# Kernel tuning notes

Measured on AMD Instinct MI355X. Metric: run time of the kernel, lower is better.

The kernel has to match this reference:

```python
import jax, jax.numpy as jnp
import numpy as np

B, C, H, W = 16, 128, 64, 64
NH = 8
HD = C // NH          # head dim == pos_embed_dim
WIN = 5               # relative-position window
OUT = 512             # out_dim of the final 1x1 projection


def _dwconv(x, w, pad):
    """Depthwise 2D conv, x: (N, Cin, H, W), w: (Cin, 1, kh, kw)."""
    return jax.lax.conv_general_dilated(
        x, w, window_strides=(1, 1), padding=[(pad, pad), (pad, pad)],
        dimension_numbers=('NCHW', 'OIHW', 'NCHW'),
        feature_group_count=x.shape[1])


def setup_inputs() -> dict:
    key = jax.random.key(0)
    ks = jax.random.split(key, 6)
    src = jax.random.normal(ks[0], (B, C, H, W), jnp.float32)
    cpe_w = jax.random.normal(ks[1], (C, 1, 3, 3), jnp.float32) * 0.1
    qkv_w = jax.random.normal(ks[2], (3 * C, C), jnp.float32) * (1.0 / np.sqrt(C))
    rel_pos = jax.random.normal(ks[3], (HD, WIN, WIN), jnp.float32) * 0.02
    conv1d_w = jax.random.normal(ks[4], (3,), jnp.float32) * 0.5
    out_w = jax.random.normal(ks[5], (OUT, 2 * C), jnp.float32) * (1.0 / np.sqrt(2 * C))
    return dict(src=src, cpe_w=cpe_w, qkv_w=qkv_w, rel_pos=rel_pos,
                conv1d_w=conv1d_w, out_w=out_w)


def reference(src, cpe_w, qkv_w, rel_pos, conv1d_w, out_w):
    scaling = HD ** (-0.5)
    feature_raw = src

    # CPE: depthwise 3x3 conv residual
    s = _dwconv(src, cpe_w, 1) + src

    # 1x1 QKV conv == channel GEMM
    qkv = jnp.einsum('oc,bchw->bohw', qkv_w, s)          # (B, 3C, H, W)
    q, k, v = jnp.split(qkv, 3, axis=1)                  # each (B, C, H, W)

    q = q.reshape(B * NH, HD, H, W)
    k = k.reshape(B * NH, HD, H, W)
    v = v.reshape(B * NH, HD, H, W)

    N = H * W
    kf = jax.nn.softmax(k.reshape(B * NH, HD, N), axis=-1)   # softmax over spatial
    vf = v.reshape(B * NH, HD, N)
    content_lambda = jnp.einsum('bin,bon->bio', kf, vf)      # (B*NH, HD, HD)
    qf = q.reshape(B * NH, HD, N) * scaling
    content_output = jnp.einsum('bin,bio->bon', qf, content_lambda)
    content_output = content_output.reshape(B * NH, HD, H, W)

    # relative-position lambda: depthwise 5x5 conv of v with rel_pos_embed
    position_lambda = _dwconv(v, rel_pos[:, None, :, :], WIN // 2)
    position_output = q * position_lambda

    result1 = (content_output + position_output).reshape(B, C, H, W)

    # ECA-style channel attention on the raw input
    pool = jnp.mean(feature_raw, axis=(2, 3))                # (B, C)
    xp = jnp.pad(pool, ((0, 0), (1, 1)))
    ca = jax.nn.sigmoid(conv1d_w[0] * xp[:, :-2]
                        + conv1d_w[1] * xp[:, 1:-1]
                        + conv1d_w[2] * xp[:, 2:])           # (B, C)
    result2 = feature_raw * ca[:, :, None, None]

    cat = jnp.concatenate([result1, result2], axis=1)       # (B, 2C, H, W)
    return jnp.einsum('oc,bchw->bohw', out_w, cat)           # (B, OUT, H, W)
```

## Files before the change

### kernel.cpp

```cpp
#include <hip/hip_runtime.h>
#include <hip/hip_bf16.h>
#include <math.h>

#define Bb   16
#define Cc   128
#define Hh   64
#define Wwid 64
#define Nn   4096
#define NHh  8
#define HDd  16
#define BHh  128
#define TCc  384
#define OUTc 512
#define KK2  256

typedef _Float16 f16x8 __attribute__((ext_vector_type(8)));
typedef float    f32x4 __attribute__((ext_vector_type(4)));

__device__ __forceinline__ ushort f2h_bits(float f) {
    _Float16 h = (_Float16)f;
    ushort u;
    __builtin_memcpy(&u, &h, 2);
    return u;
}
__device__ __forceinline__ float h2f_bits(ushort u) {
    _Float16 h;
    __builtin_memcpy(&h, &u, 2);
    return (float)h;
}

__global__ void cvt_weights(const float* __restrict__ a, int na,
                            const float* __restrict__ b2, int nb,
                            ushort* __restrict__ ya, ushort* __restrict__ yb) {
    int i = blockIdx.x * 256 + threadIdx.x;
    if (i < na) ya[i] = f2h_bits(a[i]);
    else if (i < na + nb) yb[i - na] = f2h_bits(b2[i - na]);
}

__global__ void __launch_bounds__(256) cpe_pool_kernel(const float* __restrict__ src,
                                                       const float* __restrict__ cpe_w,
                                                       ushort* __restrict__ s,
                                                       float* __restrict__ pool) {
    int bc = blockIdx.x;
    int c  = bc & (Cc - 1);
    const float* sp = src + (size_t)bc * Nn;
    __shared__ float pl[66 * 66];
    __shared__ float red[256];
    int t = threadIdx.x;
    for (int i = t; i < 66 * 66; i += 256) pl[i] = 0.f;
    __syncthreads();
    float lsum = 0.f;
    for (int i = t; i < Nn / 4; i += 256) {
        float4 v4 = ((const float4*)sp)[i];
        lsum += v4.x + v4.y + v4.z + v4.w;
        int e = i * 4, y = e >> 6, x = e & 63;
        float* d = &pl[(y + 1) * 66 + x + 1];
        d[0] = v4.x; d[1] = v4.y; d[2] = v4.z; d[3] = v4.w;
    }
    red[t] = lsum;
    float w[9];
#pragma unroll
    for (int k = 0; k < 9; k++) w[k] = cpe_w[c * 9 + k];
    __syncthreads();
    for (int s2 = 128; s2 > 0; s2 >>= 1) {
        if (t < s2) red[t] += red[t + s2];
        __syncthreads();
    }
    if (t == 0) pool[bc] = red[0] * (1.0f / Nn);
    int x = t & 63, ys = (t >> 6) * 16;
    float r[3][3];
#pragma unroll
    for (int k = 0; k < 2; k++)
#pragma unroll
        for (int j = 0; j < 3; j++) r[k][j] = pl[(ys + k) * 66 + x + j];
    ushort* dst = s + (size_t)bc * Nn;
#pragma unroll
    for (int yy = 0; yy < 16; yy++) {
        int y = ys + yy;
#pragma unroll
        for (int j = 0; j < 3; j++) r[2][j] = pl[(y + 2) * 66 + x + j];
        float acc = r[1][1];
#pragma unroll
        for (int k = 0; k < 3; k++)
#pragma unroll
            for (int j = 0; j < 3; j++) acc += r[k][j] * w[k * 3 + j];
        dst[y * 64 + x] = f2h_bits(acc);
#pragma unroll
        for (int j = 0; j < 3; j++) { r[0][j] = r[1][j]; r[1][j] = r[2][j]; }
    }
}

__global__ void ca_kernel(const float* __restrict__ pool,
                          const float* __restrict__ w3,
                          float* __restrict__ ca) {
    int i = blockIdx.x * 256 + threadIdx.x;
    if (i >= Bb * Cc) return;
    int c = i & (Cc - 1);
    float left  = (c == 0)        ? 0.f : pool[i - 1];
    float mid   = pool[i];
    float right = (c == Cc - 1)   ? 0.f : pool[i + 1];
    float v = w3[0] * left + w3[1] * mid + w3[2] * right;
    ca[i] = 1.f / (1.f + expf(-v));
}

__global__ void transpose_s(const ushort* __restrict__ s, ushort* __restrict__ sT) {
    int bz = blockIdx.z;
    int c0 = blockIdx.y * 64;
    int n0 = blockIdx.x * 64;
    __shared__ ushort t[64][68];
    int nn = threadIdx.x & 63, c4 = threadIdx.x >> 6;
    const ushort* sp = s + ((size_t)bz * Cc + c0) * Nn + n0;
#pragma unroll
    for (int p = 0; p < 16; p++) {
        int cc = p * 4 + c4;
        t[cc][nn] = sp[(size_t)cc * Nn + nn];
    }
    __syncthreads();
    int cw = threadIdx.x & 63, n4 = threadIdx.x >> 6;
    ushort* dp = sT + ((size_t)bz * Nn + n0) * Cc + c0;
#pragma unroll
    for (int p = 0; p < 16; p++) {
        int n = p * 4 + n4;
        dp[(size_t)n * Cc + cw] = t[cw][n];
    }
}

template<int K, int M>
__global__ void __launch_bounds__(256) gemm_tn(const ushort* __restrict__ A,
                                               const ushort* __restrict__ Bt,
                                               float* __restrict__ C) {
    const int bz = blockIdx.z;
    const int m0 = blockIdx.y * 128;
    const int n0 = blockIdx.x * 128;
    __shared__ __align__(16) ushort Al[128 * 32];
    __shared__ __align__(16) ushort Bl[128 * 32];
    const int tid  = threadIdx.x;
    const int wave = tid >> 6, lane = tid & 63;
    const int r = lane & 15, q = lane >> 4;
    const int wr = wave >> 1, wc = wave & 1;

    const ushort* Ag = A + (size_t)m0 * K;
    const ushort* Bg = Bt + ((size_t)bz * Nn + n0) * K;

    f32x4 acc[4][4] = {};

    for (int k0 = 0; k0 < K; k0 += 32) {
#pragma unroll
        for (int p = 0; p < 2; p++) {
            int seg = p * 4 + wave;
            int idx = seg * 64 + lane;
            int row = idx >> 2, ch = idx & 3;
            const ushort* ga = Ag + (size_t)row * K + k0 + ch * 8;
            const ushort* gb = Bg + (size_t)row * K + k0 + ch * 8;
            __builtin_amdgcn_global_load_lds(
                (const __attribute__((address_space(1))) void*)(const void*)ga,
                (__attribute__((address_space(3))) void*)(void*)(Al + seg * 512),
                16, 0, 0);
            __builtin_amdgcn_global_load_lds(
                (const __attribute__((address_space(1))) void*)(const void*)gb,
                (__attribute__((address_space(3))) void*)(void*)(Bl + seg * 512),
                16, 0, 0);
        }
        __syncthreads();

        const ushort* Apt = Al + (size_t)(wr * 64 + r) * 32 + q * 8;
        const ushort* Bpt = Bl + (size_t)(wc * 64 + r) * 32 + q * 8;
        f16x8 af[4], bf[4];
#pragma unroll
        for (int i = 0; i < 4; i++) af[i] = *(const f16x8*)(Apt + i * 16 * 32);
#pragma unroll
        for (int j = 0; j < 4; j++) bf[j] = *(const f16x8*)(Bpt + j * 16 * 32);
#pragma unroll
        for (int i = 0; i < 4; i++)
#pragma unroll
            for (int j = 0; j < 4; j++)
                acc[i][j] = __builtin_amdgcn_mfma_f32_16x16x32_f16(af[i], bf[j], acc[i][j], 0, 0, 0);
        __syncthreads();
    }

    float* Cp = C + ((size_t)bz * M + m0 + wr * 64) * Nn + n0 + wc * 64;
#pragma unroll
    for (int i = 0; i < 4; i++)
#pragma unroll
        for (int j = 0; j < 4; j++)
#pragma unroll
            for (int e = 0; e < 4; e++)
                Cp[(size_t)(i * 16 + q * 4 + e) * Nn + j * 16 + r] = acc[i][j][e];
}

__global__ void krowstat(const float* __restrict__ qkv,
                         float* __restrict__ mx, float* __restrict__ irs) {
    int row = blockIdx.x;
    int b = row >> 7, c = row & (Cc - 1);
    const float* p = qkv + (size_t)b * TCc * Nn + (size_t)(Cc + c) * Nn;
    int t = threadIdx.x;
    __shared__ float red[256];
    float m = -1e30f;
    float vals[16];
#pragma unroll
    for (int j = 0; j < 16; j++) {
        vals[j] = p[t + j * 256];
        m = fmaxf(m, vals[j]);
    }
    red[t] = m; __syncthreads();
    for (int s2 = 128; s2 > 0; s2 >>= 1) {
        if (t < s2) red[t] = fmaxf(red[t], red[t + s2]);
        __syncthreads();
    }
    m = red[0]; __syncthreads();
    float sum = 0.f;
#pragma unroll
    for (int j = 0; j < 16; j++) sum += __expf(vals[j] - m);
    red[t] = sum; __syncthreads();
    for (int s2 = 128; s2 > 0; s2 >>= 1) {
        if (t < s2) red[t] += red[t + s2];
        __syncthreads();
    }
    if (t == 0) { mx[row] = m; irs[row] = 1.f / red[0]; }
}

__global__ void __launch_bounds__(256) lambda_mfma(const float* __restrict__ qkv,
                                                   const float* __restrict__ mx,
                                                   const float* __restrict__ irs,
                                                   float* __restrict__ lamP) {
    int bh   = blockIdx.x >> 1;
    int half = blockIdx.x & 1;
    int b = bh >> 3, h = bh & 7;
    int wave = threadIdx.x >> 6, lane = threadIdx.x & 63;
    int r = lane & 15, q = lane >> 4;
    const float* kf = qkv + (size_t)b * TCc * Nn + (size_t)(Cc + h * HDd) * Nn;
    const float* vf = qkv + (size_t)b * TCc * Nn + (size_t)(2 * Cc + h * HDd) * Nn;
    float mrow = mx[b * Cc + h * HDd + r];

    f32x4 acc = {};
    int nbase = half * 2048 + wave * 512;
#pragma unroll 4
    for (int s = 0; s < 16; s++) {
        int n = nbase + s * 32 + q * 8;
        float4 ka = *(const float4*)(kf + (size_t)r * Nn + n);
        float4 kb = *(const float4*)(kf + (size_t)r * Nn + n + 4);
        float4 va = *(const float4*)(vf + (size_t)r * Nn + n);
        float4 vb = *(const float4*)(vf + (size_t)r * Nn + n + 4);
        f16x8 af, bf;
        af[0] = (_Float16)__expf(ka.x - mrow);
        af[1] = (_Float16)__expf(ka.y - mrow);
        af[2] = (_Float16)__expf(ka.z - mrow);
        af[3] = (_Float16)__expf(ka.w - mrow);
        af[4] = (_Float16)__expf(kb.x - mrow);
        af[5] = (_Float16)__expf(kb.y - mrow);
        af[6] = (_Float16)__expf(kb.z - mrow);
        af[7] = (_Float16)__expf(kb.w - mrow);
        bf[0] = (_Float16)va.x; bf[1] = (_Float16)va.y;
        bf[2] = (_Float16)va.z; bf[3] = (_Float16)va.w;
        bf[4] = (_Float16)vb.x; bf[5] = (_Float16)vb.y;
        bf[6] = (_Float16)vb.z; bf[7] = (_Float16)vb.w;
        acc = __builtin_amdgcn_mfma_f32_16x16x32_f16(af, bf, acc, 0, 0, 0);
    }

    __shared__ float red[4][256];
#pragma unroll
    for (int e = 0; e < 4; e++) red[wave][lane * 4 + e] = acc[e];
    __syncthreads();
    if (wave == 0) {
#pragma unroll
        for (int e = 0; e < 4; e++) {
            float v = red[0][lane * 4 + e] + red[1][lane * 4 + e]
                    + red[2][lane * 4 + e] + red[3][lane * 4 + e];
            int row = q * 4 + e;
            v *= irs[b * Cc + h * HDd + row];
            lamP[(size_t)half * (BHh * 256) + bh * 256 + row * 16 + r] = v;
        }
    }
}

__global__ void __launch_bounds__(256) poslam_kernel(const float* __restrict__ qkv,
                                                     const float* __restrict__ rel,
                                                     ushort* __restrict__ pos) {
    int bc = blockIdx.x;
    int b  = bc >> 7, c = bc & (Cc - 1);
    const float* vp = qkv + (size_t)b * TCc * Nn + (size_t)(2 * Cc + c) * Nn;
    __shared__ float pl[68 * 68];
    int t = threadIdx.x;
    for (int i = t; i < 68 * 68; i += 256) pl[i] = 0.f;
    __syncthreads();
    for (int i = t; i < Nn / 4; i += 256) {
        float4 v4 = ((const float4*)vp)[i];
        int e = i * 4, y = e >> 6, x = e & 63;
        float* d = &pl[(y + 2) * 68 + x + 2];
        d[0] = v4.x; d[1] = v4.y; d[2] = v4.z; d[3] = v4.w;
    }
    float w[25];
#pragma unroll
    for (int k = 0; k < 25; k++) w[k] = rel[(c & (HDd - 1)) * 25 + k];
    __syncthreads();
    int x = t & 63, ys = (t >> 6) * 16;
    float r[5][5];
#pragma unroll
    for (int k = 0; k < 4; k++)
#pragma unroll
        for (int j = 0; j < 5; j++) r[k][j] = pl[(ys + k) * 68 + x + j];
    ushort* dst = pos + (size_t)bc * Nn;
#pragma unroll
    for (int yy = 0; yy < 16; yy++) {
        int y = ys + yy;
#pragma unroll
        for (int j = 0; j < 5; j++) r[4][j] = pl[(y + 4) * 68 + x + j];
        float acc = 0.f;
#pragma unroll
        for (int k = 0; k < 5; k++)
#pragma unroll
            for (int j = 0; j < 5; j++) acc += r[k][j] * w[k * 5 + j];
        dst[y * 64 + x] = f2h_bits(acc);
#pragma unroll
        for (int k = 0; k < 4; k++)
#pragma unroll
            for (int j = 0; j < 5; j++) r[k][j] = r[k + 1][j];
    }
}

__global__ void combine_kernel(const float* __restrict__ qkv,
                               const float* __restrict__ lamP,
                               const ushort* __restrict__ pos,
                               ushort* __restrict__ catT) {
    int bh   = blockIdx.x >> 4;
    int tile = blockIdx.x & 15;
    int n = tile * 256 + threadIdx.x;
    int b = bh >> 3, h = bh & 7;
    __shared__ float lam_s[256];
    lam_s[threadIdx.x] = lamP[bh * 256 + threadIdx.x]
                       + lamP[(size_t)(BHh * 256) + bh * 256 + threadIdx.x];
    __syncthreads();
    const float* qp = qkv + (size_t)b * TCc * Nn + (size_t)(h * HDd) * Nn;
    float qv[16];
#pragma unroll
    for (int i = 0; i < 16; i++) qv[i] = qp[(size_t)i * Nn + n];
    const ushort* pp = pos + ((size_t)b * Cc + h * HDd) * Nn;
    float vals[16];
#pragma unroll
    for (int o = 0; o < 16; o++) {
        float co = 0.f;
#pragma unroll
        for (int i2 = 0; i2 < 16; i2++) co += qv[i2] * lam_s[i2 * 16 + o];
        vals[o] = co * 0.25f + qv[o] * h2f_bits(pp[(size_t)o * Nn + n]);
    }
    uint up[8];
#pragma unroll
    for (int o2 = 0; o2 < 8; o2++)
        up[o2] = (uint)f2h_bits(vals[2 * o2]) | ((uint)f2h_bits(vals[2 * o2 + 1]) << 16);
    uint4* dst = (uint4*)(catT + ((size_t)b * Nn + n) * KK2 + h * HDd);
    dst[0] = make_uint4(up[0], up[1], up[2], up[3]);
    dst[1] = make_uint4(up[4], up[5], up[6], up[7]);
}

__global__ void eca_cat(const float* __restrict__ src, const float* __restrict__ ca,
                        ushort* __restrict__ catT) {
    int bz = blockIdx.z, c0 = blockIdx.y * 64, n0 = blockIdx.x * 64;
    __shared__ ushort t[64][68];
    int nn = threadIdx.x & 63, c4 = threadIdx.x >> 6;
    const float* sp  = src + ((size_t)bz * Cc + c0) * Nn + n0;
    const float* cap = ca + bz * Cc + c0;
#pragma unroll
    for (int p = 0; p < 16; p++) {
        int cc = p * 4 + c4;
        t[cc][nn] = f2h_bits(sp[(size_t)cc * Nn + nn] * cap[cc]);
    }
    __syncthreads();
    int cw = threadIdx.x & 63, n4 = threadIdx.x >> 6;
    ushort* dp = catT + ((size_t)bz * Nn + n0) * KK2 + Cc + c0;
#pragma unroll
    for (int p = 0; p < 16; p++) {
        int n = p * 4 + n4;
        dp[(size_t)n * KK2 + cw] = t[cw][n];
    }
}

extern "C" void kernel_launch(void* const* d_in, const int* in_sizes, int n_in,
                              void* d_out, int out_size, void* d_ws, size_t ws_size,
                              hipStream_t stream) {
    const float* src      = (const float*)d_in[0];
    const float* cpe_w    = (const float*)d_in[1];
    const float* qkv_w    = (const float*)d_in[2];
    const float* rel_pos  = (const float*)d_in[3];
    const float* conv1d_w = (const float*)d_in[4];
    const float* out_w    = (const float*)d_in[5];
    float* out = (float*)d_out;

    char* ws = (char*)d_ws;
    float*  qkv   = (float*)ws;                                  ws += (size_t)Bb * TCc * Nn * 4;
    ushort* pos   = (ushort*)ws;                                 ws += (size_t)Bb * Cc * Nn * 2;
    ushort* catT  = (ushort*)ws;                                 ws += (size_t)Bb * Nn * KK2 * 2;
    ushort* sT    = (ushort*)ws;                                 ws += (size_t)Bb * Nn * Cc * 2;
    ushort* s16   = (ushort*)catT;
    float*  lamP  = (float*)ws;                                  ws += (size_t)2 * BHh * HDd * HDd * 4;
    float*  pool  = (float*)ws;                                  ws += Bb * Cc * 4;
    float*  ca    = (float*)ws;                                  ws += Bb * Cc * 4;
    float*  mx    = (float*)ws;                                  ws += Bb * Cc * 4;
    float*  irs   = (float*)ws;                                  ws += Bb * Cc * 4;
    ushort* wq16  = (ushort*)ws;                                 ws += (size_t)TCc * Cc * 2;
    ushort* wo16  = (ushort*)ws;                                 ws += (size_t)OUTc * KK2 * 2;

    {
        int na = TCc * Cc, nb = OUTc * KK2;
        cvt_weights<<<(na + nb + 255) / 256, 256, 0, stream>>>(qkv_w, na, out_w, nb, wq16, wo16);
    }
    cpe_pool_kernel<<<Bb * Cc, 256, 0, stream>>>(src, cpe_w, s16, pool);
    ca_kernel<<<(Bb * Cc + 255) / 256, 256, 0, stream>>>(pool, conv1d_w, ca);
    {
        dim3 g(Nn / 64, Cc / 64, Bb);
        transpose_s<<<g, 256, 0, stream>>>(s16, sT);
    }
    {
        dim3 g(Nn / 128, TCc / 128, Bb);
        gemm_tn<Cc, TCc><<<g, 256, 0, stream>>>(wq16, sT, qkv);
    }
    krowstat<<<Bb * Cc, 256, 0, stream>>>(qkv, mx, irs);
    lambda_mfma<<<2 * BHh, 256, 0, stream>>>(qkv, mx, irs, lamP);
    poslam_kernel<<<Bb * Cc, 256, 0, stream>>>(qkv, rel_pos, pos);
    combine_kernel<<<BHh * (Nn / 256), 256, 0, stream>>>(qkv, lamP, pos, catT);
    {
        dim3 g(Nn / 64, Cc / 64, Bb);
        eca_cat<<<g, 256, 0, stream>>>(src, ca, catT);
    }
    {
        dim3 g(Nn / 128, OUTc / 128, Bb);
        gemm_tn<KK2, OUTc><<<g, 256, 0, stream>>>(wo16, catT, out);
    }
}
```

Before: 284.5 us.

## Fuse transposes and ECA scaling into GEMM B-tile loads, full-M blocks

Removes the transpose_s and eca_cat kernels. The QKV GEMM now reads the channel-major fp16 activation directly and transposes it into LDS, and the output GEMM reads the attention part from a compact N-major buffer while scaling an fp16 copy of src by ca on the fly. Each GEMM block now covers the full M dimension (384 or 512 rows, with 768 or 1024 threads), so every B tile is loaded only once instead of once per M tile. The cost is scattered 2-byte LDS stores that may cause bank conflicts, very large blocks with low occupancy, and an extra fp16 copy of src written in the CPE kernel.

```diff
diff --git a/kernel.cpp b/kernel.cpp
--- a/kernel.cpp
+++ b/kernel.cpp
@@ -40,6 +40,7 @@
 __global__ void __launch_bounds__(256) cpe_pool_kernel(const float* __restrict__ src,
                                                        const float* __restrict__ cpe_w,
                                                        ushort* __restrict__ s,
+                                                       ushort* __restrict__ src16,
                                                        float* __restrict__ pool) {
     int bc = blockIdx.x;
     int c  = bc & (Cc - 1);
@@ -50,9 +51,13 @@
     for (int i = t; i < 66 * 66; i += 256) pl[i] = 0.f;
     __syncthreads();
     float lsum = 0.f;
+    ushort* s16p = src16 + (size_t)bc * Nn;
     for (int i = t; i < Nn / 4; i += 256) {
         float4 v4 = ((const float4*)sp)[i];
         lsum += v4.x + v4.y + v4.z + v4.w;
+        ushort4 h4 = make_ushort4(f2h_bits(v4.x), f2h_bits(v4.y),
+                                  f2h_bits(v4.z), f2h_bits(v4.w));
+        *(ushort4*)(s16p + i * 4) = h4;
         int e = i * 4, y = e >> 6, x = e & 63;
         float* d = &pl[(y + 1) * 66 + x + 1];
         d[0] = v4.x; d[1] = v4.y; d[2] = v4.z; d[3] = v4.w;
@@ -103,63 +108,68 @@
     ca[i] = 1.f / (1.f + expf(-v));
 }
 
-__global__ void transpose_s(const ushort* __restrict__ s, ushort* __restrict__ sT) {
-    int bz = blockIdx.z;
-    int c0 = blockIdx.y * 64;
-    int n0 = blockIdx.x * 64;
-    __shared__ ushort t[64][68];
-    int nn = threadIdx.x & 63, c4 = threadIdx.x >> 6;
-    const ushort* sp = s + ((size_t)bz * Cc + c0) * Nn + n0;
-#pragma unroll
-    for (int p = 0; p < 16; p++) {
-        int cc = p * 4 + c4;
-        t[cc][nn] = sp[(size_t)cc * Nn + nn];
-    }
-    __syncthreads();
-    int cw = threadIdx.x & 63, n4 = threadIdx.x >> 6;
-    ushort* dp = sT + ((size_t)bz * Nn + n0) * Cc + c0;
-#pragma unroll
-    for (int p = 0; p < 16; p++) {
-        int n = p * 4 + n4;
-        dp[(size_t)n * Cc + cw] = t[cw][n];
-    }
-}
-
-template<int K, int M>
-__global__ void __launch_bounds__(256) gemm_tn(const ushort* __restrict__ A,
-                                               const ushort* __restrict__ Bt,
-                                               float* __restrict__ C) {
+template<int K, int M, int MODE>
+__global__ void __launch_bounds__(M / 64 * 128) gemm_fused(
+        const ushort* __restrict__ A,
+        const ushort* __restrict__ B1,
+        const ushort* __restrict__ B2,
+        const float*  __restrict__ ca,
+        float* __restrict__ C) {
     const int bz = blockIdx.z;
-    const int m0 = blockIdx.y * 128;
     const int n0 = blockIdx.x * 128;
-    __shared__ __align__(16) ushort Al[128 * 32];
+    constexpr int NW = M / 64 * 2;
+    __shared__ __align__(16) ushort Al[M * 32];
     __shared__ __align__(16) ushort Bl[128 * 32];
-    const int tid  = threadIdx.x;
+    const int tid = threadIdx.x;
     const int wave = tid >> 6, lane = tid & 63;
     const int r = lane & 15, q = lane >> 4;
     const int wr = wave >> 1, wc = wave & 1;
-
-    const ushort* Ag = A + (size_t)m0 * K;
-    const ushort* Bg = Bt + ((size_t)bz * Nn + n0) * K;
+    const int sc = tid >> 4;
+    const int sn = (tid & 15) * 8;
 
     f32x4 acc[4][4] = {};
 
     for (int k0 = 0; k0 < K; k0 += 32) {
 #pragma unroll
         for (int p = 0; p < 2; p++) {
-            int seg = p * 4 + wave;
+            int seg = p * NW + wave;
             int idx = seg * 64 + lane;
             int row = idx >> 2, ch = idx & 3;
-            const ushort* ga = Ag + (size_t)row * K + k0 + ch * 8;
-            const ushort* gb = Bg + (size_t)row * K + k0 + ch * 8;
             __builtin_amdgcn_global_load_lds(
-                (const __attribute__((address_space(1))) void*)(const void*)ga,
-                (__attribute__((address_space(3))) void*)(void*)(Al + seg * 512),
+                (const __attribute__((address_space(1))) void*)(const void*)(A + (size_t)row * K + k0 + ch * 8),
+                (__attribute__((address_space(3))) void*)(void*)(Al + idx * 8),
                 16, 0, 0);
-            __builtin_amdgcn_global_load_lds(
-                (const __attribute__((address_space(1))) void*)(const void*)gb,
-                (__attribute__((address_space(3))) void*)(void*)(Bl + seg * 512),
-                16, 0, 0);
+        }
+        if constexpr (MODE == 0) {
+            if (tid < 512) {
+                const ushort* gp = B1 + ((size_t)bz * K + k0 + sc) * Nn + n0 + sn;
+                ushort v[8];
+                *(uint4*)v = *(const uint4*)gp;
+#pragma unroll
+                for (int i = 0; i < 8; i++) Bl[(sn + i) * 32 + sc] = v[i];
+            }
+        } else {
+            if (k0 < 128) {
+                if (wave < 8) {
+                    int idx = wave * 64 + lane;
+                    int row = idx >> 2, ch = idx & 3;
+                    __builtin_amdgcn_global_load_lds(
+                        (const __attribute__((address_space(1))) void*)(const void*)(B1 + ((size_t)bz * Nn + n0 + row) * 128 + k0 + ch * 8),
+                        (__attribute__((address_space(3))) void*)(void*)(Bl + idx * 8),
+                        16, 0, 0);
+                }
+            } else {
+                if (tid < 512) {
+                    int c = k0 - 128 + sc;
+                    float cav = ca[bz * Cc + c];
+                    const ushort* gp = B2 + ((size_t)bz * Cc + c) * Nn + n0 + sn;
+                    ushort v[8];
+                    *(uint4*)v = *(const uint4*)gp;
+#pragma unroll
+                    for (int i = 0; i < 8; i++)
+                        Bl[(sn + i) * 32 + sc] = f2h_bits(h2f_bits(v[i]) * cav);
+                }
+            }
         }
         __syncthreads();
 
@@ -178,7 +188,7 @@
         __syncthreads();
     }
 
-    float* Cp = C + ((size_t)bz * M + m0 + wr * 64) * Nn + n0 + wc * 64;
+    float* Cp = C + ((size_t)bz * M + wr * 64) * Nn + n0 + wc * 64;
 #pragma unroll
     for (int i = 0; i < 4; i++)
 #pragma unroll
@@ -321,7 +331,7 @@
 __global__ void combine_kernel(const float* __restrict__ qkv,
                                const float* __restrict__ lamP,
                                const ushort* __restrict__ pos,
-                               ushort* __restrict__ catT) {
+                               ushort* __restrict__ attnT) {
     int bh   = blockIdx.x >> 4;
     int tile = blockIdx.x & 15;
     int n = tile * 256 + threadIdx.x;
@@ -347,31 +357,9 @@
 #pragma unroll
     for (int o2 = 0; o2 < 8; o2++)
         up[o2] = (uint)f2h_bits(vals[2 * o2]) | ((uint)f2h_bits(vals[2 * o2 + 1]) << 16);
-    uint4* dst = (uint4*)(catT + ((size_t)b * Nn + n) * KK2 + h * HDd);
+    uint4* dst = (uint4*)(attnT + ((size_t)b * Nn + n) * Cc + h * HDd);
     dst[0] = make_uint4(up[0], up[1], up[2], up[3]);
     dst[1] = make_uint4(up[4], up[5], up[6], up[7]);
-}
-
-__global__ void eca_cat(const float* __restrict__ src, const float* __restrict__ ca,
-                        ushort* __restrict__ catT) {
-    int bz = blockIdx.z, c0 = blockIdx.y * 64, n0 = blockIdx.x * 64;
-    __shared__ ushort t[64][68];
-    int nn = threadIdx.x & 63, c4 = threadIdx.x >> 6;
-    const float* sp  = src + ((size_t)bz * Cc + c0) * Nn + n0;
-    const float* cap = ca + bz * Cc + c0;
-#pragma unroll
-    for (int p = 0; p < 16; p++) {
-        int cc = p * 4 + c4;
-        t[cc][nn] = f2h_bits(sp[(size_t)cc * Nn + nn] * cap[cc]);
-    }
-    __syncthreads();
-    int cw = threadIdx.x & 63, n4 = threadIdx.x >> 6;
-    ushort* dp = catT + ((size_t)bz * Nn + n0) * KK2 + Cc + c0;
-#pragma unroll
-    for (int p = 0; p < 16; p++) {
-        int n = p * 4 + n4;
-        dp[(size_t)n * KK2 + cw] = t[cw][n];
-    }
 }
 
 extern "C" void kernel_launch(void* const* d_in, const int* in_sizes, int n_in,
@@ -388,9 +376,9 @@
     char* ws = (char*)d_ws;
     float*  qkv   = (float*)ws;                                  ws += (size_t)Bb * TCc * Nn * 4;
     ushort* pos   = (ushort*)ws;                                 ws += (size_t)Bb * Cc * Nn * 2;
-    ushort* catT  = (ushort*)ws;                                 ws += (size_t)Bb * Nn * KK2 * 2;
-    ushort* sT    = (ushort*)ws;                                 ws += (size_t)Bb * Nn * Cc * 2;
-    ushort* s16   = (ushort*)catT;
+    ushort* attnT = (ushort*)ws;                                 ws += (size_t)Bb * Nn * Cc * 2;
+    ushort* s16   = (ushort*)ws;                                 ws += (size_t)Bb * Cc * Nn * 2;
+    ushort* src16 = (ushort*)ws;                                 ws += (size_t)Bb * Cc * Nn * 2;
     float*  lamP  = (float*)ws;                                  ws += (size_t)2 * BHh * HDd * HDd * 4;
     float*  pool  = (float*)ws;                                  ws += Bb * Cc * 4;
     float*  ca    = (float*)ws;                                  ws += Bb * Cc * 4;
@@ -403,26 +391,18 @@
         int na = TCc * Cc, nb = OUTc * KK2;
         cvt_weights<<<(na + nb + 255) / 256, 256, 0, stream>>>(qkv_w, na, out_w, nb, wq16, wo16);
     }
-    cpe_pool_kernel<<<Bb * Cc, 256, 0, stream>>>(src, cpe_w, s16, pool);
+    cpe_pool_kernel<<<Bb * Cc, 256, 0, stream>>>(src, cpe_w, s16, src16, pool);
     ca_kernel<<<(Bb * Cc + 255) / 256, 256, 0, stream>>>(pool, conv1d_w, ca);
     {
-        dim3 g(Nn / 64, Cc / 64, Bb);
-        transpose_s<<<g, 256, 0, stream>>>(s16, sT);
-    }
-    {
-        dim3 g(Nn / 128, TCc / 128, Bb);
-        gemm_tn<Cc, TCc><<<g, 256, 0, stream>>>(wq16, sT, qkv);
+        dim3 g(Nn / 128, 1, Bb);
+        gemm_fused<Cc, TCc, 0><<<g, TCc / 64 * 128, 0, stream>>>(wq16, s16, nullptr, nullptr, qkv);
     }
     krowstat<<<Bb * Cc, 256, 0, stream>>>(qkv, mx, irs);
     lambda_mfma<<<2 * BHh, 256, 0, stream>>>(qkv, mx, irs, lamP);
     poslam_kernel<<<Bb * Cc, 256, 0, stream>>>(qkv, rel_pos, pos);
-    combine_kernel<<<BHh * (Nn / 256), 256, 0, stream>>>(qkv, lamP, pos, catT);
+    combine_kernel<<<BHh * (Nn / 256), 256, 0, stream>>>(qkv, lamP, pos, attnT);
     {
-        dim3 g(Nn / 64, Cc / 64, Bb);
-        eca_cat<<<g, 256, 0, stream>>>(src, ca, catT);
-    }
-    {
-        dim3 g(Nn / 128, OUTc / 128, Bb);
-        gemm_tn<KK2, OUTc><<<g, 256, 0, stream>>>(wo16, catT, out);
-    }
-}
+        dim3 g(Nn / 128, 1, Bb);
+        gemm_fused<KK2, OUTc, 1><<<g, OUTc / 64 * 128, 0, stream>>>(wo16, attnT, src16, ca, out);
+    }
+}
```

After: 303.4 us. +6.6%, slower.
